# Performance work log

Measured on AMD Instinct MI355X. Metric: run time of the kernel, lower is better.

The kernel has to match this reference:

```python
import jax, jax.numpy as jnp
import numpy as np

SOS = 1  # letter2index['<sos>']
EOS = 0  # letter2index['<eos>'] (embedding padding_idx)

B, T, KV, E, H, V, L = 64, 2048, 128, 256, 512, 30, 256


def _lstm_cell(x, h, c, W_ih, W_hh, b_ih, b_hh):
    # PyTorch LSTMCell: gates ordered (i, f, g, o)
    gates = x @ W_ih.T + b_ih + h @ W_hh.T + b_hh
    i, f, g, o = jnp.split(gates, 4, axis=-1)
    c_new = jax.nn.sigmoid(f) * c + jax.nn.sigmoid(i) * jnp.tanh(g)
    h_new = jax.nn.sigmoid(o) * jnp.tanh(c_new)
    return h_new, c_new


def setup_inputs() -> dict:
    root = jax.random.key(0)
    ks = jax.random.split(root, 16)

    key = jax.random.normal(ks[0], (B, T, KV), dtype=jnp.float32)
    value = jax.random.normal(ks[1], (B, T, KV), dtype=jnp.float32)
    encoder_len = jax.random.randint(ks[2], (B,), 1, T + 1)
    y = jax.random.randint(ks[3], (B, L), 0, V)

    def w(k, shape, fan_in):
        return jax.random.normal(k, shape, dtype=jnp.float32) / np.sqrt(fan_in)

    emb_weight = w(ks[4], (V, E), E).at[EOS].set(0.0)  # padding_idx row zeroed
    in1 = E + KV
    W_ih1 = w(ks[5], (4 * H, in1), in1)
    W_hh1 = w(ks[6], (4 * H, H), H)
    b_ih1 = jnp.zeros((4 * H,), jnp.float32)
    b_hh1 = jnp.zeros((4 * H,), jnp.float32)
    W_ih2 = w(ks[7], (4 * KV, H), H)
    W_hh2 = w(ks[8], (4 * KV, KV), KV)
    b_ih2 = jnp.zeros((4 * KV,), jnp.float32)
    b_hh2 = jnp.zeros((4 * KV,), jnp.float32)
    out_bias = jnp.zeros((V,), jnp.float32)

    return dict(key=key, value=value, encoder_len=encoder_len, y=y,
                emb_weight=emb_weight,
                W_ih1=W_ih1, W_hh1=W_hh1, b_ih1=b_ih1, b_hh1=b_hh1,
                W_ih2=W_ih2, W_hh2=W_hh2, b_ih2=b_ih2, b_hh2=b_hh2,
                out_bias=out_bias)


def reference(key, value, encoder_len, y, emb_weight,
              W_ih1, W_hh1, b_ih1, b_hh1,
              W_ih2, W_hh2, b_ih2, b_hh2, out_bias):
    Bq, Tq, d_k = key.shape
    mask = jnp.arange(Tq)[None, :] >= encoder_len[:, None]  # (B, T) True = padded
    scale = 1.0 / np.sqrt(d_k).astype(np.float32)

    # Teacher forcing rate 1.0 in train mode: step i uses embed(SOS) at i=0,
    # embed(y[:, i-1]) afterwards.
    ids = jnp.concatenate([jnp.full((Bq, 1), SOS, dtype=y.dtype), y[:, :-1]], axis=1)
    embeds = emb_weight[ids]               # (B, L, E)
    embeds_t = jnp.swapaxes(embeds, 0, 1)  # (L, B, E)

    h_dim = W_hh1.shape[1]
    kv_dim = W_hh2.shape[1]
    init = (jnp.zeros((Bq, h_dim), key.dtype), jnp.zeros((Bq, h_dim), key.dtype),
            jnp.zeros((Bq, kv_dim), key.dtype), jnp.zeros((Bq, kv_dim), key.dtype),
            value.mean(axis=1))  # initial context

    def step(carry, char_embed):
        h1, c1, h2, c2, context = carry
        x = jnp.concatenate([char_embed, context], axis=1)
        h1, c1 = _lstm_cell(x, h1, c1, W_ih1, W_hh1, b_ih1, b_hh1)
        h2, c2 = _lstm_cell(h1, h2, c2, W_ih2, W_hh2, b_ih2, b_hh2)
        query = h2                                             # (B, KV)
        energy = jnp.einsum('bd,btd->bt', query, key) * scale  # (B, T)
        energy = jnp.where(mask, -1e9, energy)
        attn = jax.nn.softmax(energy, axis=1)
        ctx = jnp.einsum('bt,btd->bd', attn, value)            # (B, KV)
        logits = jnp.concatenate([query, ctx], axis=1) @ emb_weight.T + out_bias
        return (h1, c1, h2, c2, ctx), (logits, attn[0])

    _, (preds, attn_plot) = jax.lax.scan(step, init, embeds_t)
    predictions = jnp.swapaxes(preds, 0, 1)  # (B, L, V)
    return predictions, attn_plot            # attn_plot: (L, T), batch element 0
```

## Files before the change

### kernel.cpp

```cpp
#include <hip/hip_runtime.h>

#define NB 256
#define NT 1024

#define BB   64
#define TTS  2048
#define DKV  128
#define EEM  256
#define HH1  512
#define VVV  30
#define LLS  256
#define SOS_ID 1
#define SCALE_F 0.088388347648318447f

#define OFF_PM    0
#define OFF_PS    256
#define OFF_PCTX  512
#define OFF_WSE   33280
#define OFF_EMBT  35328
#define OFF_H1    68096
#define OFF_C1    133632
#define OFF_H2R   166400
#define OFF_H2T   182784
#define OFF_C2    199168
#define OFF_BAR   207360
#define OFF_KBF   212992
#define OFF_VBF   8601600
#define WS_NEED_BYTES 67960832ull
#define PRED_SZ   491520

struct Params {
  const float* key; const float* value;
  const int* enc_len; const int* y;
  const float* emb;
  const float* Wih1; const float* Whh1; const float* bih1; const float* bhh1;
  const float* Wih2; const float* Whh2; const float* bih2; const float* bhh2;
  const float* obias;
  float* out; float* ws;
};

struct SMEM {
  union {
    struct {
      float ctxT[8192];
      union { float wt[8192]; float red[8192]; } u;
    } a;
    struct { float wm[16]; float wS[16]; float wctx[2048]; } c;
  };
};

__device__ __forceinline__ float sigm(float x) { return 1.f / (1.f + __expf(-x)); }
__device__ __forceinline__ float tanh_f(float x) {
  float t = __expf(-2.f * fabsf(x));
  float r = (1.f - t) / (1.f + t);
  return x < 0.f ? -r : r;
}
__device__ __forceinline__ unsigned bfr(float f) {
  unsigned u = __float_as_uint(f);
  return (u + 0x7FFFu + ((u >> 16) & 1u)) >> 16;
}
__device__ __forceinline__ float blo(unsigned u) { return __uint_as_float(u << 16); }
__device__ __forceinline__ float bhi(unsigned u) { return __uint_as_float(u & 0xffff0000u); }

__device__ __forceinline__ void gbar(unsigned* base, unsigned expect) {
  __syncthreads();
  if (threadIdx.x == 0) {
    __builtin_amdgcn_fence(__ATOMIC_RELEASE, "agent");
    const int grp = blockIdx.x >> 3;
    unsigned* gcnt = base + grp * 32;
    if (__hip_atomic_fetch_add(gcnt, 1u, __ATOMIC_RELAXED, __HIP_MEMORY_SCOPE_AGENT) == 7u) {
      unsigned* mcnt = base + 1024;
      if (__hip_atomic_fetch_add(mcnt, 1u, __ATOMIC_RELAXED, __HIP_MEMORY_SCOPE_AGENT) == 31u) {
        __hip_atomic_store(mcnt, 0u, __ATOMIC_RELAXED, __HIP_MEMORY_SCOPE_AGENT);
        #pragma unroll
        for (int gg = 0; gg < 32; ++gg)
          __hip_atomic_store(base + gg * 32, 0u, __ATOMIC_RELAXED, __HIP_MEMORY_SCOPE_AGENT);
        __builtin_amdgcn_fence(__ATOMIC_RELEASE, "agent");
        #pragma unroll
        for (int gg = 0; gg < 32; ++gg)
          __hip_atomic_store(base + 2048 + gg * 32, expect, __ATOMIC_RELAXED, __HIP_MEMORY_SCOPE_AGENT);
      }
    }
    unsigned* mygen = base + 2048 + grp * 32;
    int guard = 0;
    while ((int)(__hip_atomic_load(mygen, __ATOMIC_RELAXED, __HIP_MEMORY_SCOPE_AGENT) - expect) < 0) {
      __builtin_amdgcn_s_sleep(8);
      if (++guard > 10000000) break;
    }
    __builtin_amdgcn_fence(__ATOMIC_ACQUIRE, "agent");
  }
  __syncthreads();
}

__device__ __forceinline__ void mac8x4(float acc[8][4], const float* wt, int k, float4 x4) {
  float4 wa = *(const float4*)(wt + k*8);
  float4 wb = *(const float4*)(wt + k*8 + 4);
  float wr[8] = {wa.x, wa.y, wa.z, wa.w, wb.x, wb.y, wb.z, wb.w};
  float xr[4] = {x4.x, x4.y, x4.z, x4.w};
  #pragma unroll
  for (int r = 0; r < 8; ++r)
    #pragma unroll
    for (int c = 0; c < 4; ++c)
      acc[r][c] += wr[r] * xr[c];
}

__device__ __forceinline__ void gate_reduce_store(float acc[8][4], float* red, int tid) {
  #pragma unroll
  for (int r = 0; r < 8; ++r) {
    #pragma unroll
    for (int c = 0; c < 4; ++c) {
      float v = acc[r][c];
      v += __shfl_xor(v, 16);
      v += __shfl_xor(v, 32);
      acc[r][c] = v;
    }
  }
  int wv = tid >> 6, b0 = tid & 15;
  if ((tid & 63) < 16) {
    #pragma unroll
    for (int r = 0; r < 8; ++r)
      *(float4*)(red + wv*512 + r*64 + b0*4) =
        make_float4(acc[r][0], acc[r][1], acc[r][2], acc[r][3]);
  }
}

__device__ __forceinline__ void attn_merge_tail(float m, float S, float ca[8],
                                                float* pm, float* pS, float* pctx,
                                                SMEM* sm, int bj, int tid) {
  const int lane = tid & 63, w = tid >> 6;
  const int sub = lane & 15, grp = lane >> 4;
  #pragma unroll
  for (int off = 16; off <= 32; off <<= 1) {
    float mo = __shfl_xor(m, off);
    float So = __shfl_xor(S, off);
    float M2 = fmaxf(m, mo);
    float a0 = __expf(m - M2), a1 = __expf(mo - M2);
    S = S*a0 + So*a1;
    #pragma unroll
    for (int d = 0; d < 8; ++d)
      ca[d] = ca[d]*a0 + __shfl_xor(ca[d], off)*a1;
    m = M2;
  }
  if (lane == 0) { sm->c.wm[w] = m; sm->c.wS[w] = S; }
  if (grp == 0) {
    *(float4*)(sm->c.wctx + w*DKV + sub*8)     = make_float4(ca[0],ca[1],ca[2],ca[3]);
    *(float4*)(sm->c.wctx + w*DKV + sub*8 + 4) = make_float4(ca[4],ca[5],ca[6],ca[7]);
  }
  __syncthreads();
  if (tid < DKV) {
    int d = tid;
    float M = -1e30f;
    #pragma unroll
    for (int ww = 0; ww < 16; ++ww) M = fmaxf(M, sm->c.wm[ww]);
    float Z = 0.f, acc2 = 0.f;
    #pragma unroll
    for (int ww = 0; ww < 16; ++ww) {
      float aw = __expf(sm->c.wm[ww] - M);
      Z += aw * sm->c.wS[ww];
      acc2 += aw * sm->c.wctx[ww*DKV + d];
    }
    pctx[d*256 + bj] = acc2;
    if (d == 0) { pm[bj] = M; pS[bj] = Z; }
  }
}

__device__ void attn_mean(const Params& p, float* pm, float* pS, float* pctx,
                          SMEM* sm, int bj, int tid) {
  const int lane = tid & 63, w = tid >> 6;
  const int b = bj >> 2, s = bj & 3;
  const int sub = lane & 15, grp = lane >> 4;
  const int q = 4*w + s;
  const int r0 = q*4 + grp;
  float S = 0.f;
  float ca[8] = {0.f,0.f,0.f,0.f,0.f,0.f,0.f,0.f};
  const float* vb = p.value + (size_t)b * TTS * DKV;
  #pragma unroll
  for (int j = 0; j < 8; ++j) {
    int t = r0 + 256*j;
    const float* vp = vb + (size_t)t * DKV + sub*8;
    float4 va = *(const float4*)vp;
    float4 vb4 = *(const float4*)(vp + 4);
    S += 1.f;
    ca[0]+=va.x;  ca[1]+=va.y;  ca[2]+=va.z;  ca[3]+=va.w;
    ca[4]+=vb4.x; ca[5]+=vb4.y; ca[6]+=vb4.z; ca[7]+=vb4.w;
  }
  attn_merge_tail(0.f, S, ca, pm, pS, pctx, sm, bj, tid);
}

template<int NC>
__device__ __forceinline__ void attn_cluster_bf16(
    const unsigned short* kb, const unsigned short* vbp, const float* q8,
    int r0, int len, float* wsE, int b, int sub,
    float& m, float& S, float* ca) {
  uint4 kq[NC], vq[NC];
  #pragma unroll
  for (int j = 0; j < NC; ++j) {
    int t = r0 + 256*j;
    int tc = t < len ? t : len - 1;
    kq[j] = *(const uint4*)(kb + (size_t)tc*DKV);
  }
  #pragma unroll
  for (int j = 0; j < NC; ++j) {
    int t = r0 + 256*j;
    int tc = t < len ? t : len - 1;
    vq[j] = *(const uint4*)(vbp + (size_t)tc*DKV);
  }
  __builtin_amdgcn_sched_barrier(0);
  float e[NC];
  #pragma unroll
  for (int j = 0; j < NC; ++j) {
    float ep = blo(kq[j].x)*q8[0] + bhi(kq[j].x)*q8[1]
             + blo(kq[j].y)*q8[2] + bhi(kq[j].y)*q8[3]
             + blo(kq[j].z)*q8[4] + bhi(kq[j].z)*q8[5]
             + blo(kq[j].w)*q8[6] + bhi(kq[j].w)*q8[7];
    ep += __shfl_xor(ep, 1); ep += __shfl_xor(ep, 2);
    ep += __shfl_xor(ep, 4); ep += __shfl_xor(ep, 8);
    int t = r0 + 256*j;
    e[j] = (t < len) ? ep * SCALE_F : -1e30f;
    if (b == 0 && sub == 0 && t < len) wsE[t] = e[j];
  }
  m = e[0];
  #pragma unroll
  for (int j = 1; j < NC; ++j) m = fmaxf(m, e[j]);
  float pr[NC];
  #pragma unroll
  for (int j = 0; j < NC; ++j) {
    pr[j] = (e[j] > -1e29f) ? __expf(e[j] - m) : 0.f;
    S += pr[j];
  }
  #pragma unroll
  for (int j = 0; j < NC; ++j) {
    ca[0] += pr[j]*blo(vq[j].x); ca[1] += pr[j]*bhi(vq[j].x);
    ca[2] += pr[j]*blo(vq[j].y); ca[3] += pr[j]*bhi(vq[j].y);
    ca[4] += pr[j]*blo(vq[j].z); ca[5] += pr[j]*bhi(vq[j].z);
    ca[6] += pr[j]*blo(vq[j].w); ca[7] += pr[j]*bhi(vq[j].w);
  }
}

template<bool BF16>
__device__ void phase_attn_main(const Params& p, const float* qrow,
                                const unsigned short* kbf, const unsigned short* vbf,
                                float* pm, float* pS, float* pctx, float* wsE,
                                SMEM* sm, int bj, int tid) {
  const int lane = tid & 63, w = tid >> 6;
  const int b = bj >> 2, s = bj & 3;
  const int len = p.enc_len[b];
  const int sub = lane & 15, grp = lane >> 4;
  const int q = 4*w + s;
  const int r0 = q*4 + grp;
  float m = -1e30f, S = 0.f;
  float ca[8] = {0.f,0.f,0.f,0.f,0.f,0.f,0.f,0.f};
  int NJ = 0;
  { int d = len - 4*q; if (d > 0) { NJ = (d + 255) >> 8; if (NJ > 8) NJ = 8; } }
  if (NJ > 0) {
    float q8[8];
    {
      const float* qp = qrow + b*DKV + sub*8;
      float4 qa = *(const float4*)qp;
      float4 qb = *(const float4*)(qp + 4);
      q8[0]=qa.x; q8[1]=qa.y; q8[2]=qa.z; q8[3]=qa.w;
      q8[4]=qb.x; q8[5]=qb.y; q8[6]=qb.z; q8[7]=qb.w;
    }
    if constexpr (BF16) {
      const unsigned short* kb  = kbf + (size_t)(b*TTS)*DKV + sub*8;
      const unsigned short* vbp = vbf + (size_t)(b*TTS)*DKV + sub*8;
      if (NJ >= 5)
        attn_cluster_bf16<8>(kb, vbp, q8, r0, len, wsE, b, sub, m, S, ca);
      else
        attn_cluster_bf16<4>(kb, vbp, q8, r0, len, wsE, b, sub, m, S, ca);
    } else {
      float e[8];
      #pragma unroll
      for (int j = 0; j < 8; ++j) e[j] = -1e30f;
      for (int j = 0; j < NJ; ++j) {
        int t = r0 + 256*j;
        int tc = t < len ? t : len - 1;
        const float* kp = p.key + (size_t)(b*TTS + tc)*DKV + sub*8;
        float4 ka = *(const float4*)kp;
        float4 kb2 = *(const float4*)(kp + 4);
        float ep = ka.x*q8[0] + ka.y*q8[1] + ka.z*q8[2] + ka.w*q8[3]
                 + kb2.x*q8[4] + kb2.y*q8[5] + kb2.z*q8[6] + kb2.w*q8[7];
        ep += __shfl_xor(ep, 1); ep += __shfl_xor(ep, 2);
        ep += __shfl_xor(ep, 4); ep += __shfl_xor(ep, 8);
        e[j] = (t < len) ? ep * SCALE_F : -1e30f;
        if (b == 0 && sub == 0 && t < len) wsE[t] = e[j];
      }
      m = e[0];
      #pragma unroll
      for (int j = 1; j < 8; ++j) m = fmaxf(m, e[j]);
      float pr[8];
      #pragma unroll
      for (int j = 0; j < 8; ++j) {
        pr[j] = (e[j] > -1e29f) ? __expf(e[j] - m) : 0.f;
        S += pr[j];
      }
      for (int j = 0; j < NJ; ++j) {
        int t = r0 + 256*j;
        int tc = t < len ? t : len - 1;
        const float* vp = p.value + (size_t)(b*TTS + tc)*DKV + sub*8;
        float4 va = *(const float4*)vp;
        float4 vb4 = *(const float4*)(vp + 4);
        ca[0] += pr[j]*va.x;  ca[1] += pr[j]*va.y;
        ca[2] += pr[j]*va.z;  ca[3] += pr[j]*va.w;
        ca[4] += pr[j]*vb4.x; ca[5] += pr[j]*vb4.y;
        ca[6] += pr[j]*vb4.z; ca[7] += pr[j]*vb4.w;
      }
    }
  }
  attn_merge_tail(m, S, ca, pm, pS, pctx, sm, bj, tid);
}

template<bool BF16>
__global__ void
__attribute__((amdgpu_flat_work_group_size(NT, NT), amdgpu_waves_per_eu(4, 4)))
decoder_kernel(Params p) {
  const int tid = threadIdx.x;
  const int bj = blockIdx.x;
  float* ws = p.ws;
  unsigned* bar = (unsigned*)(ws + OFF_BAR);
  float* pm = ws + OFF_PM;
  float* pS = ws + OFF_PS;
  float* pctx = ws + OFF_PCTX;
  float* wsE = ws + OFF_WSE;
  float* embT0 = ws + OFF_EMBT;
  float* embT1 = ws + OFF_EMBT + EEM*BB;
  float* h1b0 = ws + OFF_H1;
  float* h1b1 = ws + OFF_H1 + HH1*BB;
  float* c1 = ws + OFF_C1;
  float* h2r0 = ws + OFF_H2R;
  float* h2r1 = ws + OFF_H2R + BB*DKV;
  float* h2t0 = ws + OFF_H2T;
  float* h2t1 = ws + OFF_H2T + DKV*BB;
  float* c2 = ws + OFF_C2;
  unsigned short* kbf = (unsigned short*)(ws + OFF_KBF);
  unsigned short* vbf = (unsigned short*)(ws + OFF_VBF);
  unsigned genc = 0;

  __shared__ SMEM sm;

  float wr1[8] = {0,0,0,0,0,0,0,0};
  if (tid < 896) {
    #pragma unroll
    for (int r = 0; r < 8; ++r) {
      int grow = (r >> 1)*HH1 + 2*bj + (r & 1);
      wr1[r] = (tid < 384) ? p.Wih1[(size_t)grow*384 + tid]
                           : p.Whh1[(size_t)grow*HH1 + (tid - 384)];
    }
  }
  float wr2[8] = {0,0,0,0,0,0,0,0};
  if (bj < 64 && tid < 640) {
    #pragma unroll
    for (int r = 0; r < 8; ++r) {
      int grow = (r >> 1)*DKV + 2*bj + (r & 1);
      wr2[r] = (tid < 512) ? p.Wih2[(size_t)grow*HH1 + tid]
                           : p.Whh2[(size_t)grow*DKV + (tid - 512)];
    }
  }
  float bsum1 = 0.f, bsum2 = 0.f;
  if (tid < 512) {
    int r = tid >> 6;
    int g1 = (r >> 1)*HH1 + 2*bj + (r & 1);
    bsum1 = p.bih1[g1] + p.bhh1[g1];
    if (bj < 64) {
      int g2 = (r >> 1)*DKV + 2*bj + (r & 1);
      bsum2 = p.bih2[g2] + p.bhh2[g2];
    }
  }

  {
    int gid = bj*NT + tid;
    for (int idx = gid; idx < (OFF_BAR - OFF_H1); idx += NB*NT) ws[OFF_H1 + idx] = 0.f;
    for (int idx = gid; idx < EEM*BB; idx += NB*NT) {
      int k = idx >> 6, b = idx & 63;
      embT0[k*64 + b] = p.emb[SOS_ID*EEM + k];
    }
    if constexpr (BF16) {
      const int NG = (BB*TTS*DKV) / 8;
      for (int g = gid; g < NG; g += NB*NT) {
        const float4* src = (const float4*)p.key + (size_t)g*2;
        float4 a = src[0], bq = src[1];
        uint4 o;
        o.x = bfr(a.x)  | (bfr(a.y)  << 16);
        o.y = bfr(a.z)  | (bfr(a.w)  << 16);
        o.z = bfr(bq.x) | (bfr(bq.y) << 16);
        o.w = bfr(bq.z) | (bfr(bq.w) << 16);
        ((uint4*)kbf)[g] = o;
      }
      for (int g = gid; g < NG; g += NB*NT) {
        const float4* src = (const float4*)p.value + (size_t)g*2;
        float4 a = src[0], bq = src[1];
        uint4 o;
        o.x = bfr(a.x)  | (bfr(a.y)  << 16);
        o.y = bfr(a.z)  | (bfr(a.w)  << 16);
        o.z = bfr(bq.x) | (bfr(bq.y) << 16);
        o.w = bfr(bq.z) | (bfr(bq.w) << 16);
        ((uint4*)vbf)[g] = o;
      }
    }
    attn_mean(p, pm, pS, pctx, &sm, bj, tid);
  }
  gbar(bar, ++genc);

  for (int i = 0; i <= LLS; ++i) {
    const int cur = i & 1;
    float* h1c = cur ? h1b1 : h1b0;
    const float* h1p = cur ? h1b0 : h1b1;
    float* h2rc = cur ? h2r1 : h2r0;
    const float* h2rp = cur ? h2r0 : h2r1;
    float* h2tc = cur ? h2t1 : h2t0;
    const float* h2tp = cur ? h2t0 : h2t1;
    const float* et = cur ? embT1 : embT0;
    float* etn = cur ? embT0 : embT1;

    {
      int b = tid & 63, dg = tid >> 6;
      float4 m4 = *(const float4*)(pm + b*4);
      float4 s4 = *(const float4*)(pS + b*4);
      float M = fmaxf(fmaxf(m4.x, m4.y), fmaxf(m4.z, m4.w));
      float a0 = __expf(m4.x - M), a1 = __expf(m4.y - M);
      float a2 = __expf(m4.z - M), a3 = __expf(m4.w - M);
      float Z = a0*s4.x + a1*s4.y + a2*s4.z + a3*s4.w;
      float iZ = 1.f / Z;
      a0 *= iZ; a1 *= iZ; a2 *= iZ; a3 *= iZ;
      #pragma unroll
      for (int jj = 0; jj < 8; ++jj) {
        int d = dg + jj*16;
        float4 c4 = *(const float4*)(pctx + d*256 + b*4);
        sm.a.ctxT[d*64 + b] = a0*c4.x + a1*c4.y + a2*c4.z + a3*c4.w;
      }
    }
    if (i < LLS && tid < 896) {
      *(float4*)(sm.a.u.wt + tid*8)     = make_float4(wr1[0], wr1[1], wr1[2], wr1[3]);
      *(float4*)(sm.a.u.wt + tid*8 + 4) = make_float4(wr1[4], wr1[5], wr1[6], wr1[7]);
    }
    __syncthreads();

    if (i < LLS) {
      {
        const int b0 = tid & 15, ks = tid >> 4;
        float acc[8][4];
        #pragma unroll
        for (int r = 0; r < 8; ++r) { acc[r][0]=0.f; acc[r][1]=0.f; acc[r][2]=0.f; acc[r][3]=0.f; }
        #pragma unroll
        for (int j = 0; j < 4; ++j) {
          int k = ks*4 + j;
          float4 x4 = *(const float4*)(et + k*64 + b0*4);
          mac8x4(acc, sm.a.u.wt, k, x4);
        }
        #pragma unroll
        for (int j = 0; j < 2; ++j) {
          int d = ks*2 + j;
          float4 x4 = *(const float4*)(sm.a.ctxT + d*64 + b0*4);
          mac8x4(acc, sm.a.u.wt, 256 + d, x4);
        }
        #pragma unroll
        for (int j = 0; j < 8; ++j) {
          int kk = ks*8 + j;
          float4 x4 = *(const float4*)(h1p + kk*64 + b0*4);
          mac8x4(acc, sm.a.u.wt, 384 + kk, x4);
        }
        __syncthreads();
        gate_reduce_store(acc, sm.a.u.red, tid);
      }
      __syncthreads();
      if (tid < 512) {
        int r = tid >> 6, b = tid & 63;
        float s = 0.f;
        #pragma unroll
        for (int w2 = 0; w2 < 16; ++w2) s += sm.a.u.red[w2*512 + r*64 + b];
        s += bsum1;
        sm.a.u.red[r*64 + b] = s;
      }
      __syncthreads();
      if (tid < 128) {
        int hh = tid >> 6, b = tid & 63;
        int h = 2*bj + hh;
        float gi = sm.a.u.red[(hh+0)*64 + b];
        float gf = sm.a.u.red[(hh+2)*64 + b];
        float gg = sm.a.u.red[(hh+4)*64 + b];
        float go = sm.a.u.red[(hh+6)*64 + b];
        float co = c1[h*64 + b];
        float cn = sigm(gf)*co + sigm(gi)*tanh_f(gg);
        float hn = sigm(go)*tanh_f(cn);
        c1[h*64 + b] = cn;
        h1c[h*64 + b] = hn;
      }
    }

    if (i >= 1) {
      if (tid >= 960) {
        int ln = tid - 960;
        int oi = bj*8 + (ln >> 3);
        int sub = ln & 7;
        if (oi < BB*VVV) {
          int b = oi / VVV, v = oi - b*VVV;
          float a = 0.f;
          if (sub < 4) {
            #pragma unroll 8
            for (int e0 = 0; e0 < 32; ++e0) {
              int e = sub*32 + e0;
              a += h2rp[b*DKV + e] * p.emb[v*EEM + e];
            }
          } else {
            #pragma unroll 8
            for (int e0 = 0; e0 < 32; ++e0) {
              int d = (sub - 4)*32 + e0;
              a += sm.a.ctxT[d*64 + b] * p.emb[v*EEM + 128 + d];
            }
          }
          a += __shfl_xor(a, 1); a += __shfl_xor(a, 2); a += __shfl_xor(a, 4);
          if (sub == 0) p.out[((size_t)b*LLS + (i-1))*VVV + v] = a + p.obias[v];
        }
      }
      if (tid >= 896 && tid < 904) {
        int t = bj*8 + (tid - 896);
        int len0 = p.enc_len[0];
        float v = 0.f;
        if (t < len0) {
          float m0 = pm[0], m1 = pm[1], m2 = pm[2], m3 = pm[3];
          float M = fmaxf(fmaxf(m0, m1), fmaxf(m2, m3));
          float Z = __expf(m0 - M)*pS[0] + __expf(m1 - M)*pS[1]
                  + __expf(m2 - M)*pS[2] + __expf(m3 - M)*pS[3];
          v = __expf(wsE[t] - M) / Z;
        }
        p.out[PRED_SZ + (size_t)(i-1)*TTS + t] = v;
      }
    }

    if (i == LLS) break;
    gbar(bar, ++genc);

    if (bj < 64) {
      if (tid < 640) {
        *(float4*)(sm.a.u.wt + tid*8)     = make_float4(wr2[0], wr2[1], wr2[2], wr2[3]);
        *(float4*)(sm.a.u.wt + tid*8 + 4) = make_float4(wr2[4], wr2[5], wr2[6], wr2[7]);
      }
      __syncthreads();
      {
        const int b0 = tid & 15, ks = tid >> 4;
        float acc[8][4];
        #pragma unroll
        for (int r = 0; r < 8; ++r) { acc[r][0]=0.f; acc[r][1]=0.f; acc[r][2]=0.f; acc[r][3]=0.f; }
        #pragma unroll
        for (int j = 0; j < 8; ++j) {
          int k = ks*8 + j;
          float4 x4 = *(const float4*)(h1c + k*64 + b0*4);
          mac8x4(acc, sm.a.u.wt, k, x4);
        }
        #pragma unroll
        for (int j = 0; j < 2; ++j) {
          int d = ks*2 + j;
          float4 x4 = *(const float4*)(h2tp + d*64 + b0*4);
          mac8x4(acc, sm.a.u.wt, 512 + d, x4);
        }
        __syncthreads();
        gate_reduce_store(acc, sm.a.u.red, tid);
      }
      __syncthreads();
      if (tid < 512) {
        int r = tid >> 6, b = tid & 63;
        float s = 0.f;
        #pragma unroll
        for (int w2 = 0; w2 < 16; ++w2) s += sm.a.u.red[w2*512 + r*64 + b];
        s += bsum2;
        sm.a.u.red[r*64 + b] = s;
      }
      __syncthreads();
      if (tid < 128) {
        int hh = tid >> 6, b = tid & 63;
        int d2 = 2*bj + hh;
        float gi = sm.a.u.red[(hh+0)*64 + b];
        float gf = sm.a.u.red[(hh+2)*64 + b];
        float gg = sm.a.u.red[(hh+4)*64 + b];
        float go = sm.a.u.red[(hh+6)*64 + b];
        float co = c2[d2*64 + b];
        float cn = sigm(gf)*co + sigm(gi)*tanh_f(gg);
        float hn = sigm(go)*tanh_f(cn);
        c2[d2*64 + b] = cn;
        h2rc[b*DKV + d2] = hn;
        h2tc[d2*64 + b] = hn;
      }
    } else if (bj < 128) {
      int sn = i + 1;
      if (sn < LLS && tid < 256) {
        int idx = (bj - 64)*256 + tid;
        int k = idx >> 6, b = idx & 63;
        int id = p.y[b*LLS + sn - 1];
        etn[k*64 + b] = p.emb[(size_t)id*EEM + k];
      }
    }
    gbar(bar, ++genc);

    phase_attn_main<BF16>(p, h2rc, kbf, vbf, pm, pS, pctx, wsE, &sm, bj, tid);
    gbar(bar, ++genc);
  }
}

__global__ void init_bar_kernel(unsigned* bar) {
  int i = blockIdx.x * blockDim.x + threadIdx.x;
  if (i < 4096) bar[i] = 0u;
}

extern "C" void kernel_launch(void* const* d_in, const int* in_sizes, int n_in,
                              void* d_out, int out_size, void* d_ws, size_t ws_size,
                              hipStream_t stream) {
  Params prm;
  prm.key     = (const float*)d_in[0];
  prm.value   = (const float*)d_in[1];
  prm.enc_len = (const int*)d_in[2];
  prm.y       = (const int*)d_in[3];
  prm.emb     = (const float*)d_in[4];
  prm.Wih1    = (const float*)d_in[5];
  prm.Whh1    = (const float*)d_in[6];
  prm.bih1    = (const float*)d_in[7];
  prm.bhh1    = (const float*)d_in[8];
  prm.Wih2    = (const float*)d_in[9];
  prm.Whh2    = (const float*)d_in[10];
  prm.bih2    = (const float*)d_in[11];
  prm.bhh2    = (const float*)d_in[12];
  prm.obias   = (const float*)d_in[13];
  prm.out = (float*)d_out;
  prm.ws  = (float*)d_ws;

  unsigned* bar = (unsigned*)((float*)d_ws + OFF_BAR);
  init_bar_kernel<<<16, 256, 0, stream>>>(bar);

  void* args[] = { &prm };
  if (ws_size >= WS_NEED_BYTES) {
    hipError_t e = hipLaunchCooperativeKernel((const void*)decoder_kernel<true>,
                                              dim3(NB), dim3(NT), args, 0, stream);
    if (e != hipSuccess) decoder_kernel<true><<<dim3(NB), dim3(NT), 0, stream>>>(prm);
  } else {
    hipError_t e = hipLaunchCooperativeKernel((const void*)decoder_kernel<false>,
                                              dim3(NB), dim3(NT), args, 0, stream);
    if (e != hipSuccess) decoder_kernel<false><<<dim3(NB), dim3(NT), 0, stream>>>(prm);
  }
}
```

Measured before the change: 18.53 ms.

## Use fence-free grid barriers with sc0/sc1 stores and prefetch K/V before barrier

Replaces two of the three per-step grid barriers with a lighter variant that skips the agent-scope release/acquire fences. Cross-block visibility of h1 and h2 is kept by writing them with sc0 sc1 global stores and reading the query back with sc0 sc1 loads, staged through shared memory. Before the barrier, each block issues dummy loads of its first bf16 key/value rows to warm the cache for the next attention phase. The attention cluster is also unified into one 8-wide predicated loop. Relying on cache-bypass bits instead of fences is a memory-ordering risk: c1/c2, h2tc and the etn embeddings are still written with plain stores and depend only on the fence-free barrier.

Result: faster. 15.69 ms (-15.3%).

```diff
diff --git a/kernel.cpp b/kernel.cpp
--- a/kernel.cpp
+++ b/kernel.cpp
@@ -29,6 +29,8 @@
 #define WS_NEED_BYTES 67960832ull
 #define PRED_SZ   491520
 
+typedef unsigned u32x4 __attribute__((ext_vector_type(4)));
+
 struct Params {
   const float* key; const float* value;
   const int* enc_len; const int* y;
@@ -45,7 +47,7 @@
       float ctxT[8192];
       union { float wt[8192]; float red[8192]; } u;
     } a;
-    struct { float wm[16]; float wS[16]; float wctx[2048]; } c;
+    struct { float wm[16]; float wS[16]; float wctx[2048]; float qh2[128]; } c;
   };
 };
 
@@ -88,6 +90,35 @@
       if (++guard > 10000000) break;
     }
     __builtin_amdgcn_fence(__ATOMIC_ACQUIRE, "agent");
+  }
+  __syncthreads();
+}
+
+__device__ __forceinline__ void gbar_light(unsigned* base, unsigned expect) {
+  asm volatile("s_waitcnt vmcnt(0)" ::: "memory");
+  __syncthreads();
+  if (threadIdx.x == 0) {
+    const int grp = blockIdx.x >> 3;
+    unsigned* gcnt = base + grp * 32;
+    if (__hip_atomic_fetch_add(gcnt, 1u, __ATOMIC_RELAXED, __HIP_MEMORY_SCOPE_AGENT) == 7u) {
+      unsigned* mcnt = base + 1024;
+      if (__hip_atomic_fetch_add(mcnt, 1u, __ATOMIC_RELAXED, __HIP_MEMORY_SCOPE_AGENT) == 31u) {
+        __hip_atomic_store(mcnt, 0u, __ATOMIC_RELAXED, __HIP_MEMORY_SCOPE_AGENT);
+        #pragma unroll
+        for (int gg = 0; gg < 32; ++gg)
+          __hip_atomic_store(base + gg * 32, 0u, __ATOMIC_RELAXED, __HIP_MEMORY_SCOPE_AGENT);
+        asm volatile("s_waitcnt vmcnt(0)" ::: "memory");
+        #pragma unroll
+        for (int gg = 0; gg < 32; ++gg)
+          __hip_atomic_store(base + 2048 + gg * 32, expect, __ATOMIC_RELAXED, __HIP_MEMORY_SCOPE_AGENT);
+      }
+    }
+    unsigned* mygen = base + 2048 + grp * 32;
+    int guard = 0;
+    while ((int)(__hip_atomic_load(mygen, __ATOMIC_RELAXED, __HIP_MEMORY_SCOPE_AGENT) - expect) < 0) {
+      __builtin_amdgcn_s_sleep(8);
+      if (++guard > 10000000) break;
+    }
   }
   __syncthreads();
 }
@@ -184,56 +215,27 @@
     ca[0]+=va.x;  ca[1]+=va.y;  ca[2]+=va.z;  ca[3]+=va.w;
     ca[4]+=vb4.x; ca[5]+=vb4.y; ca[6]+=vb4.z; ca[7]+=vb4.w;
   }
-  attn_merge_tail(0.f, S, ca, pm, pS, pctx, sm, bj, tid);
-}
-
-template<int NC>
-__device__ __forceinline__ void attn_cluster_bf16(
-    const unsigned short* kb, const unsigned short* vbp, const float* q8,
-    int r0, int len, float* wsE, int b, int sub,
-    float& m, float& S, float* ca) {
-  uint4 kq[NC], vq[NC];
-  #pragma unroll
-  for (int j = 0; j < NC; ++j) {
+  attn_merge_tail(0.f, S, ca, pm, pS, pctx, sm, b*4 + s, tid);
+}
+
+__device__ __forceinline__ void prefetch_kv(const unsigned short* kbf,
+                                            const unsigned short* vbf,
+                                            int b, int s, int len, int tid) {
+  const int lane = tid & 63, w = tid >> 6;
+  const int sub = lane & 15, grp = lane >> 4;
+  const int q = 4*w + s;
+  if (len <= q*4) return;
+  int NJ = ((len - 4*q) + 255) >> 8; if (NJ > 8) NJ = 8;
+  const int NP = NJ < 3 ? NJ : 3;
+  const int r0 = q*4 + grp;
+  const unsigned base = (unsigned)(b*TTS*DKV + sub*8) * 2u;
+  unsigned d;
+  for (int j = 0; j < NP; ++j) {
     int t = r0 + 256*j;
     int tc = t < len ? t : len - 1;
-    kq[j] = *(const uint4*)(kb + (size_t)tc*DKV);
-  }
-  #pragma unroll
-  for (int j = 0; j < NC; ++j) {
-    int t = r0 + 256*j;
-    int tc = t < len ? t : len - 1;
-    vq[j] = *(const uint4*)(vbp + (size_t)tc*DKV);
-  }
-  __builtin_amdgcn_sched_barrier(0);
-  float e[NC];
-  #pragma unroll
-  for (int j = 0; j < NC; ++j) {
-    float ep = blo(kq[j].x)*q8[0] + bhi(kq[j].x)*q8[1]
-             + blo(kq[j].y)*q8[2] + bhi(kq[j].y)*q8[3]
-             + blo(kq[j].z)*q8[4] + bhi(kq[j].z)*q8[5]
-             + blo(kq[j].w)*q8[6] + bhi(kq[j].w)*q8[7];
-    ep += __shfl_xor(ep, 1); ep += __shfl_xor(ep, 2);
-    ep += __shfl_xor(ep, 4); ep += __shfl_xor(ep, 8);
-    int t = r0 + 256*j;
-    e[j] = (t < len) ? ep * SCALE_F : -1e30f;
-    if (b == 0 && sub == 0 && t < len) wsE[t] = e[j];
-  }
-  m = e[0];
-  #pragma unroll
-  for (int j = 1; j < NC; ++j) m = fmaxf(m, e[j]);
-  float pr[NC];
-  #pragma unroll
-  for (int j = 0; j < NC; ++j) {
-    pr[j] = (e[j] > -1e29f) ? __expf(e[j] - m) : 0.f;
-    S += pr[j];
-  }
-  #pragma unroll
-  for (int j = 0; j < NC; ++j) {
-    ca[0] += pr[j]*blo(vq[j].x); ca[1] += pr[j]*bhi(vq[j].x);
-    ca[2] += pr[j]*blo(vq[j].y); ca[3] += pr[j]*bhi(vq[j].y);
-    ca[4] += pr[j]*blo(vq[j].z); ca[5] += pr[j]*bhi(vq[j].z);
-    ca[6] += pr[j]*blo(vq[j].w); ca[7] += pr[j]*bhi(vq[j].w);
+    unsigned off = base + (unsigned)tc * (DKV*2);
+    asm volatile("global_load_dword %0, %1, %2" : "=v"(d) : "v"(off), "s"(kbf));
+    asm volatile("global_load_dword %0, %1, %2" : "=v"(d) : "v"(off), "s"(vbf));
   }
 }
 
@@ -250,28 +252,81 @@
   const int r0 = q*4 + grp;
   float m = -1e30f, S = 0.f;
   float ca[8] = {0.f,0.f,0.f,0.f,0.f,0.f,0.f,0.f};
+  if constexpr (BF16) {
+    if (tid < 32) {
+      u32x4 qv;
+      asm volatile("global_load_dwordx4 %0, %1, %2 sc0 sc1"
+                   : "=v"(qv) : "v"((unsigned)(tid*16)), "s"(qrow + b*DKV));
+      asm volatile("s_waitcnt vmcnt(0)" ::: "memory");
+      *(u32x4*)&sm->c.qh2[tid*4] = qv;
+    }
+    __syncthreads();
+  }
   int NJ = 0;
   { int d = len - 4*q; if (d > 0) { NJ = (d + 255) >> 8; if (NJ > 8) NJ = 8; } }
   if (NJ > 0) {
     float q8[8];
-    {
+    if constexpr (BF16) {
+      const float* qp = sm->c.qh2 + sub*8;
+      float4 qa = *(const float4*)qp;
+      float4 qb = *(const float4*)(qp + 4);
+      q8[0]=qa.x; q8[1]=qa.y; q8[2]=qa.z; q8[3]=qa.w;
+      q8[4]=qb.x; q8[5]=qb.y; q8[6]=qb.z; q8[7]=qb.w;
+    } else {
       const float* qp = qrow + b*DKV + sub*8;
       float4 qa = *(const float4*)qp;
       float4 qb = *(const float4*)(qp + 4);
       q8[0]=qa.x; q8[1]=qa.y; q8[2]=qa.z; q8[3]=qa.w;
       q8[4]=qb.x; q8[5]=qb.y; q8[6]=qb.z; q8[7]=qb.w;
     }
+    float e[8];
+    #pragma unroll
+    for (int j = 0; j < 8; ++j) e[j] = -1e30f;
     if constexpr (BF16) {
       const unsigned short* kb  = kbf + (size_t)(b*TTS)*DKV + sub*8;
       const unsigned short* vbp = vbf + (size_t)(b*TTS)*DKV + sub*8;
-      if (NJ >= 5)
-        attn_cluster_bf16<8>(kb, vbp, q8, r0, len, wsE, b, sub, m, S, ca);
-      else
-        attn_cluster_bf16<4>(kb, vbp, q8, r0, len, wsE, b, sub, m, S, ca);
+      uint4 kq[8], vq[8];
+      #pragma unroll
+      for (int j = 0; j < 8; ++j) {
+        if (j < NJ) {
+          int t = r0 + 256*j;
+          int tc = t < len ? t : len - 1;
+          kq[j] = *(const uint4*)(kb  + (size_t)tc * DKV);
+          vq[j] = *(const uint4*)(vbp + (size_t)tc * DKV);
+        }
+      }
+      #pragma unroll
+      for (int j = 0; j < 8; ++j) {
+        if (j < NJ) {
+          float ep = blo(kq[j].x)*q8[0] + bhi(kq[j].x)*q8[1]
+                   + blo(kq[j].y)*q8[2] + bhi(kq[j].y)*q8[3]
+                   + blo(kq[j].z)*q8[4] + bhi(kq[j].z)*q8[5]
+                   + blo(kq[j].w)*q8[6] + bhi(kq[j].w)*q8[7];
+          ep += __shfl_xor(ep, 1); ep += __shfl_xor(ep, 2);
+          ep += __shfl_xor(ep, 4); ep += __shfl_xor(ep, 8);
+          int t = r0 + 256*j;
+          e[j] = (t < len) ? ep * SCALE_F : -1e30f;
+          if (b == 0 && sub == 0 && t < len) wsE[t] = e[j];
+        }
+      }
+      m = fmaxf(fmaxf(fmaxf(e[0],e[1]), fmaxf(e[2],e[3])),
+                fmaxf(fmaxf(e[4],e[5]), fmaxf(e[6],e[7])));
+      float pr[8];
+      #pragma unroll
+      for (int j = 0; j < 8; ++j) {
+        pr[j] = (e[j] > -1e29f) ? __expf(e[j] - m) : 0.f;
+        S += pr[j];
+      }
+      #pragma unroll
+      for (int j = 0; j < 8; ++j) {
+        if (j < NJ) {
+          ca[0] += pr[j]*blo(vq[j].x); ca[1] += pr[j]*bhi(vq[j].x);
+          ca[2] += pr[j]*blo(vq[j].y); ca[3] += pr[j]*bhi(vq[j].y);
+          ca[4] += pr[j]*blo(vq[j].z); ca[5] += pr[j]*bhi(vq[j].z);
+          ca[6] += pr[j]*blo(vq[j].w); ca[7] += pr[j]*bhi(vq[j].w);
+        }
+      }
     } else {
-      float e[8];
-      #pragma unroll
-      for (int j = 0; j < 8; ++j) e[j] = -1e30f;
       for (int j = 0; j < NJ; ++j) {
         int t = r0 + 256*j;
         int tc = t < len ? t : len - 1;
@@ -336,6 +391,9 @@
   unsigned short* vbf = (unsigned short*)(ws + OFF_VBF);
   unsigned genc = 0;
 
+  const int b_my = bj >> 2, s_my = bj & 3;
+  const int len_my = p.enc_len[b_my];
+
   __shared__ SMEM sm;
 
   float wr1[8] = {0,0,0,0,0,0,0,0};
@@ -483,7 +541,8 @@
         float cn = sigm(gf)*co + sigm(gi)*tanh_f(gg);
         float hn = sigm(go)*tanh_f(cn);
         c1[h*64 + b] = cn;
-        h1c[h*64 + b] = hn;
+        asm volatile("global_store_dword %0, %1, %2 sc0 sc1"
+                     :: "v"((unsigned)((h*64 + b)*4)), "v"(hn), "s"(h1c) : "memory");
       }
     }
 
@@ -528,7 +587,9 @@
     }
 
     if (i == LLS) break;
-    gbar(bar, ++genc);
+
+    if constexpr (BF16) prefetch_kv(kbf, vbf, b_my, s_my, len_my, tid);
+    gbar_light(bar, ++genc);
 
     if (bj < 64) {
       if (tid < 640) {
@@ -577,8 +638,9 @@
         float cn = sigm(gf)*co + sigm(gi)*tanh_f(gg);
         float hn = sigm(go)*tanh_f(cn);
         c2[d2*64 + b] = cn;
-        h2rc[b*DKV + d2] = hn;
         h2tc[d2*64 + b] = hn;
+        asm volatile("global_store_dword %0, %1, %2 sc0 sc1"
+                     :: "v"((unsigned)((b*DKV + d2)*4)), "v"(hn), "s"(h2rc) : "memory");
       }
     } else if (bj < 128) {
       int sn = i + 1;
@@ -589,7 +651,7 @@
         etn[k*64 + b] = p.emb[(size_t)id*EEM + k];
       }
     }
-    gbar(bar, ++genc);
+    gbar_light(bar, ++genc);
 
     phase_attn_main<BF16>(p, h2rc, kbf, vbf, pm, pS, pctx, wsE, &sm, bj, tid);
     gbar(bar, ++genc);
```
